# Optimization experiments

Measured on AMD Instinct MI355X. Metric: run time of the kernel, lower is better.

## Reference

```python
import jax, jax.numpy as jnp
import numpy as np

D_MODEL = 4096
N_TYPES = 6  # fixed event_types list in the module


def setup_inputs() -> dict:
    key = jax.random.key(0)
    ks = jax.random.split(key, 7)
    E, B, d = 131072, 16384, D_MODEL
    return {
        "event_type": jax.random.randint(ks[0], (E,), 0, N_TYPES),
        "confidence": jax.random.uniform(ks[1], (E,), jnp.float32),
        "location": jax.random.uniform(ks[2], (E, 2), jnp.float32) * jnp.array([640.0, 480.0], jnp.float32),
        "batch_idx": jax.random.randint(ks[3], (E,), 0, B),
        "batch_size": B,
        "type_emb": jax.random.normal(ks[4], (N_TYPES, d // 4), jnp.float32),
        "W1": jax.random.normal(ks[5], (d // 2, d // 4 + 3), jnp.float32) / np.sqrt(d // 4 + 3).astype(np.float32),
        "b1": jnp.zeros((d // 2,), jnp.float32),
        "W2": jax.random.normal(ks[6], (d, d // 2), jnp.float32) / np.sqrt(d // 2).astype(np.float32),
        "b2": jnp.zeros((d,), jnp.float32),
    }


def reference(event_type, confidence, location, batch_idx, batch_size, type_emb, W1, b1, W2, b2):
    E = confidence.shape[0]
    B = batch_size
    # per-batch-slot max confidence (empty slots -> -inf)
    seg_max = jax.ops.segment_max(confidence, batch_idx, num_segments=B)
    is_top = confidence == seg_max[batch_idx]
    # first event attaining the max (matches torch's max-over-list semantics)
    cand = jnp.where(is_top, jnp.arange(E), E)
    top_idx = jnp.full((B,), E, dtype=cand.dtype).at[batch_idx].min(cand)
    has_event = top_idx < E
    safe_idx = jnp.where(has_event, top_idx, 0)

    emb = type_emb[event_type[safe_idx]]                 # [B, d/4]
    c = confidence[safe_idx][:, None]                    # [B, 1]
    loc = location[safe_idx] / jnp.array([640.0, 480.0], jnp.float32)  # [B, 2]
    feats = jnp.concatenate([emb, c, loc], axis=-1)      # [B, d/4 + 3]

    h = jax.nn.relu(feats @ W1.T + b1)                   # [B, d/2]
    out = h @ W2.T + b2                                  # [B, d]
    return jnp.where(has_event[:, None], out, jnp.zeros((), out.dtype))
```

## Files before the change

kernel.cpp:

```cpp
#include <hip/hip_runtime.h>
#include <hip/hip_bf16.h>

#define NT 6
#define BM 256
#define BN 256
#define BK 64
#define SLOT_S 32768
#define AH1 8192
#define BOFF_A 16384
#define BH1 24576

typedef __attribute__((ext_vector_type(16))) float f32x16;
typedef __attribute__((ext_vector_type(8))) short bf16x8;

__device__ __forceinline__ short f2bf(float f) {
    __hip_bfloat16 h = __float2bfloat16(f);
    return (short)__builtin_bit_cast(unsigned short, h);
}

__global__ void k_segmax(const float* __restrict__ conf,
                         const int* __restrict__ bidx,
                         unsigned long long* __restrict__ packed, int E) {
    int i = blockIdx.x * blockDim.x + threadIdx.x;
    if (i >= E) return;
    unsigned cb = __float_as_uint(conf[i]);
    unsigned long long p = ((unsigned long long)cb << 32) | (unsigned)(~(unsigned)i);
    atomicMax(&packed[bidx[i]], p);
}

__global__ void k_base(const float* __restrict__ emb, const float* __restrict__ W1,
                       const float* __restrict__ b1, float* __restrict__ base,
                       float* __restrict__ vecs, int d2, int d4) {
    int gw = (blockIdx.x * blockDim.x + threadIdx.x) >> 6;
    int lane = threadIdx.x & 63;
    int t = gw / d2, n = gw % d2;
    const float* e = emb + (size_t)t * d4;
    const float* w = W1 + (size_t)n * (d4 + 3);
    float s = 0.f;
    for (int k = lane; k < d4; k += 64) s += e[k] * w[k];
#pragma unroll
    for (int m = 32; m; m >>= 1) s += __shfl_xor(s, m);
    if (lane == 0) {
        base[gw] = s + b1[n];
        if (t == 0) {
            vecs[n]          = w[d4];
            vecs[d2 + n]     = w[d4 + 1];
            vecs[2 * d2 + n] = w[d4 + 2];
        }
    }
}

__global__ void k_w2cast(const float* __restrict__ W2, short* __restrict__ W2b, long n) {
    long i = ((long)blockIdx.x * blockDim.x + threadIdx.x) * 8;
    if (i >= n) return;
    bf16x8 v;
#pragma unroll
    for (int j = 0; j < 8; ++j) v[j] = f2bf(W2[i + j]);
    *(bf16x8*)(W2b + i) = v;
}

__global__ void k_h(const unsigned long long* __restrict__ packed,
                    const int* __restrict__ etype, const float* __restrict__ loc,
                    const float* __restrict__ base, const float* __restrict__ vecs,
                    float* __restrict__ mask, short* __restrict__ h, int d2) {
    int b = blockIdx.x;
    int tid = threadIdx.x;
    unsigned long long p = packed[b];
    bool has = (p != 0ULL);
    float conf = 0.f, lx = 0.f, ly = 0.f;
    int t = 0;
    if (has) {
        unsigned idx = ~(unsigned)(p & 0xFFFFFFFFu);
        conf = __uint_as_float((unsigned)(p >> 32));
        t  = etype[idx];
        lx = loc[2 * (size_t)idx]     * (1.0f / 640.0f);
        ly = loc[2 * (size_t)idx + 1] * (1.0f / 480.0f);
    }
    if (tid == 0) mask[b] = has ? 1.0f : 0.0f;
    const float* bs = base + (size_t)t * d2;
    const float* cv = vecs;
    const float* xv = vecs + d2;
    const float* yv = vecs + 2 * d2;
    int n0 = tid * 8;
    bf16x8 v;
#pragma unroll
    for (int j = 0; j < 8; ++j) {
        int n = n0 + j;
        float g = bs[n] + conf * cv[n] + lx * xv[n] + ly * yv[n];
        g = fmaxf(g, 0.f);
        v[j] = has ? f2bf(g) : (short)0;
    }
    *(bf16x8*)(h + (size_t)b * d2 + n0) = v;
}


#define GLL(src, dst) __builtin_amdgcn_global_load_lds(                      \
    (const __attribute__((address_space(1))) void*)(src),                    \
    (__attribute__((address_space(3))) void*)(dst), 16, 0, 0)

#define ST_AH0(ws, kt) { GLL(pA + (size_t)(kt) * 64, (ws) + dst1);           \
                         GLL(pA + (size_t)64 * K + (kt) * 64, (ws) + dst2); }
#define ST_AH1(ws, kt) { GLL(pA + (size_t)128 * K + (kt) * 64, (ws) + AH1 + dst1); \
                         GLL(pA + (size_t)192 * K + (kt) * 64, (ws) + AH1 + dst2); }
#define ST_BH0(ws, kt) { GLL(pB + (size_t)(kt) * 64, (ws) + BOFF_A + dst1);  \
                         GLL(pB + (size_t)64 * K + (kt) * 64, (ws) + BOFF_A + dst2); }
#define ST_BH1(ws, kt) { GLL(pB + (size_t)128 * K + (kt) * 64, (ws) + BH1 + dst1); \
                         GLL(pB + (size_t)192 * K + (kt) * 64, (ws) + BH1 + dst2); }

__global__ __launch_bounds__(512, 2)
void k_gemm(const short* __restrict__ A, const short* __restrict__ Bm,
            const float* __restrict__ b2, const float* __restrict__ mask,
            float* __restrict__ C, int M, int N, int K, int nbn) {
    __shared__ __align__(16) short lds[2 * SLOT_S];

    int tid = threadIdx.x;
    int lane = tid & 63;
    int wave = tid >> 6;
    int wr = wave >> 2, wc = wave & 3;

    int bid = blockIdx.x;
    int wg = (bid & 7) * ((int)gridDim.x >> 3) + (bid >> 3);
    int bm = wg / nbn, bn = wg % nbn;
    int row0 = bm * BM, col0 = bn * BN;

    int r1 = tid >> 3;
    int pg = tid & 7;
    int cg = pg ^ (r1 & 7);
    const short* pA = A + (size_t)(row0 + r1) * K + cg * 8;
    const short* pB = Bm + (size_t)(col0 + r1) * K + cg * 8;
    int dst1 = tid * 8;
    int dst2 = 4096 + tid * 8;

    int l31 = lane & 31, kh = lane >> 5;
    int kx7 = l31 & 7;
    int aBase = (wr * 128 + l31) * 64;
    int bBase = BOFF_A + (wc * 64 + l31) * 64;
    int coff[4];
#pragma unroll
    for (int s = 0; s < 4; ++s) coff[s] = ((2 * s + kh) ^ kx7) * 8;

    f32x16 acc[4][2] = {};
    bf16x8 aA[4][4], bB[2][4];

    int KT = K / BK;

    ST_AH0(lds, 0); ST_BH0(lds, 0); ST_BH1(lds, 0); ST_AH1(lds, 0);
    asm volatile("s_waitcnt vmcnt(0)" ::: "memory");
    __builtin_amdgcn_s_barrier();

#pragma unroll 1
    for (int t = 0; t < KT; ++t) {
        const short* sl = lds + (t & 1) * SLOT_S;
        short* wsl = lds + ((t + 1) & 1) * SLOT_S;

#pragma unroll
        for (int mi = 0; mi < 4; ++mi)
#pragma unroll
            for (int s = 0; s < 4; ++s)
                aA[mi][s] = *(const bf16x8*)(sl + aBase + mi * 2048 + coff[s]);
#pragma unroll
        for (int ni = 0; ni < 2; ++ni)
#pragma unroll
            for (int s = 0; s < 4; ++s)
                bB[ni][s] = *(const bf16x8*)(sl + bBase + ni * 2048 + coff[s]);

        if (t < KT - 1) {
            ST_AH0(wsl, t + 1); ST_BH0(wsl, t + 1);
            ST_BH1(wsl, t + 1); ST_AH1(wsl, t + 1);
        }

        __builtin_amdgcn_s_setprio(1);
#pragma unroll
        for (int mi = 0; mi < 4; ++mi)
#pragma unroll
            for (int ni = 0; ni < 2; ++ni)
#pragma unroll
                for (int s = 0; s < 4; ++s)
                    acc[mi][ni] = __builtin_amdgcn_mfma_f32_32x32x16_bf16(
                        aA[mi][s], bB[ni][s], acc[mi][ni], 0, 0, 0);
        __builtin_amdgcn_s_setprio(0);

        if (t < KT - 1) {
            asm volatile("s_waitcnt vmcnt(0)" ::: "memory");
            __builtin_amdgcn_s_barrier();
        }
    }

#pragma unroll
    for (int mi = 0; mi < 4; ++mi) {
        int rb = row0 + wr * 128 + mi * 32 + 4 * kh;
#pragma unroll
        for (int q = 0; q < 4; ++q) {
#pragma unroll
            for (int j = 0; j < 4; ++j) {
                int r = rb + 8 * q + j;
                float mk = mask[r];
#pragma unroll
                for (int ni = 0; ni < 2; ++ni) {
                    int c = col0 + wc * 64 + ni * 32 + l31;
                    C[(size_t)r * N + c] = (acc[mi][ni][q * 4 + j] + b2[c]) * mk;
                }
            }
        }
    }
}

extern "C" void kernel_launch(void* const* d_in, const int* in_sizes, int n_in,
                              void* d_out, int out_size, void* d_ws, size_t ws_size,
                              hipStream_t stream) {
    const int* etype   = (const int*)d_in[0];
    const float* conf  = (const float*)d_in[1];
    const float* loc   = (const float*)d_in[2];
    const int* bidx    = (const int*)d_in[3];
    const float* emb   = (const float*)d_in[5];
    const float* W1    = (const float*)d_in[6];
    const float* b1    = (const float*)d_in[7];
    const float* W2    = (const float*)d_in[8];
    const float* b2    = (const float*)d_in[9];
    float* out = (float*)d_out;

    int E  = in_sizes[0];
    int d2 = in_sizes[7];
    int d  = in_sizes[9];
    int d4 = in_sizes[5] / NT;
    int B  = out_size / d;

    char* ws = (char*)d_ws;
    unsigned long long* packed = (unsigned long long*)ws;
    float* mask = (float*)(ws + (size_t)B * 8);
    float* base = mask + B;
    float* vecs = base + NT * d2;
    short* w2b  = (short*)(vecs + 3 * d2);
    short* h    = w2b + (size_t)d * d2;

    hipMemsetAsync(packed, 0, (size_t)B * 8, stream);
    k_segmax<<<(E + 255) / 256, 256, 0, stream>>>(conf, bidx, packed, E);
    k_base<<<(NT * d2) / 4, 256, 0, stream>>>(emb, W1, b1, base, vecs, d2, d4);
    long nw2 = (long)d * d2;
    k_w2cast<<<(int)(nw2 / 8 / 256), 256, 0, stream>>>(W2, w2b, nw2);
    k_h<<<B, 256, 0, stream>>>(packed, etype, loc, base, vecs, mask, h, d2);
    int nbm = B / BM, nbn = d / BN;
    k_gemm<<<dim3(nbm * nbn), dim3(512), 0, stream>>>(h, w2b, b2, mask, out, B, d, d2, nbn);
}
```

Measured before the change: 330.9 us.

## Store GEMM tiles in MFMA fragment order in LDS instead of XOR swizzle

Changes how global_load_lds places the A and B tiles in shared memory. Each wave's 64 lanes now write a contiguous 32-row by 16-column fragment, so the MFMA operand reads become linear lane*8 offsets with no XOR swizzle arithmetic and no bank conflicts. It also drops the s_setprio raise around the MFMA block. Global loads now read 64 bytes per row per wave instead of full 128-byte row segments, which may reduce coalescing efficiency.

```diff
diff --git a/kernel.cpp b/kernel.cpp
--- a/kernel.cpp
+++ b/kernel.cpp
@@ -6,9 +6,7 @@
 #define BN 256
 #define BK 64
 #define SLOT_S 32768
-#define AH1 8192
-#define BOFF_A 16384
-#define BH1 24576
+#define B_BASE 16384
 
 typedef __attribute__((ext_vector_type(16))) float f32x16;
 typedef __attribute__((ext_vector_type(8))) short bf16x8;
@@ -98,14 +96,16 @@
     (const __attribute__((address_space(1))) void*)(src),                    \
     (__attribute__((address_space(3))) void*)(dst), 16, 0, 0)
 
-#define ST_AH0(ws, kt) { GLL(pA + (size_t)(kt) * 64, (ws) + dst1);           \
-                         GLL(pA + (size_t)64 * K + (kt) * 64, (ws) + dst2); }
-#define ST_AH1(ws, kt) { GLL(pA + (size_t)128 * K + (kt) * 64, (ws) + AH1 + dst1); \
-                         GLL(pA + (size_t)192 * K + (kt) * 64, (ws) + AH1 + dst2); }
-#define ST_BH0(ws, kt) { GLL(pB + (size_t)(kt) * 64, (ws) + BOFF_A + dst1);  \
-                         GLL(pB + (size_t)64 * K + (kt) * 64, (ws) + BOFF_A + dst2); }
-#define ST_BH1(ws, kt) { GLL(pB + (size_t)128 * K + (kt) * 64, (ws) + BH1 + dst1); \
-                         GLL(pB + (size_t)192 * K + (kt) * 64, (ws) + BH1 + dst2); }
+#define ST_A(ws, kt) {                                                       \
+    GLL(pA + (size_t)(kt) * 64,               (ws) + dstG);                  \
+    GLL(pA + (size_t)64  * K + (kt) * 64,     (ws) + 4096  + dstG);          \
+    GLL(pA + (size_t)128 * K + (kt) * 64,     (ws) + 8192  + dstG);          \
+    GLL(pA + (size_t)192 * K + (kt) * 64,     (ws) + 12288 + dstG); }
+#define ST_B(ws, kt) {                                                       \
+    GLL(pB + (size_t)(kt) * 64,               (ws) + B_BASE + dstG);         \
+    GLL(pB + (size_t)64  * K + (kt) * 64,     (ws) + B_BASE + 4096  + dstG); \
+    GLL(pB + (size_t)128 * K + (kt) * 64,     (ws) + B_BASE + 8192  + dstG); \
+    GLL(pB + (size_t)192 * K + (kt) * 64,     (ws) + B_BASE + 12288 + dstG); }
 
 __global__ __launch_bounds__(512, 2)
 void k_gemm(const short* __restrict__ A, const short* __restrict__ Bm,
@@ -123,28 +123,22 @@
     int bm = wg / nbn, bn = wg % nbn;
     int row0 = bm * BM, col0 = bn * BN;
 
-    int r1 = tid >> 3;
-    int pg = tid & 7;
-    int cg = pg ^ (r1 & 7);
-    const short* pA = A + (size_t)(row0 + r1) * K + cg * 8;
-    const short* pB = Bm + (size_t)(col0 + r1) * K + cg * 8;
-    int dst1 = tid * 8;
-    int dst2 = 4096 + tid * 8;
+    int rA = ((tid >> 8) << 5) + (tid & 31);
+    int cA = (((tid >> 6) & 3) << 1) + ((tid >> 5) & 1);
+    const short* pA = A + (size_t)(row0 + rA) * K + cA * 8;
+    const short* pB = Bm + (size_t)(col0 + rA) * K + cA * 8;
+    int dstG = tid * 8;
 
     int l31 = lane & 31, kh = lane >> 5;
-    int kx7 = l31 & 7;
-    int aBase = (wr * 128 + l31) * 64;
-    int bBase = BOFF_A + (wc * 64 + l31) * 64;
-    int coff[4];
-#pragma unroll
-    for (int s = 0; s < 4; ++s) coff[s] = ((2 * s + kh) ^ kx7) * 8;
+    int aBase = (wr * 4) * 2048 + lane * 8;
+    int bBase = B_BASE + (wc * 2) * 2048 + lane * 8;
 
     f32x16 acc[4][2] = {};
     bf16x8 aA[4][4], bB[2][4];
 
     int KT = K / BK;
 
-    ST_AH0(lds, 0); ST_BH0(lds, 0); ST_BH1(lds, 0); ST_AH1(lds, 0);
+    ST_A(lds, 0); ST_B(lds, 0);
     asm volatile("s_waitcnt vmcnt(0)" ::: "memory");
     __builtin_amdgcn_s_barrier();
 
@@ -157,19 +151,15 @@
         for (int mi = 0; mi < 4; ++mi)
 #pragma unroll
             for (int s = 0; s < 4; ++s)
-                aA[mi][s] = *(const bf16x8*)(sl + aBase + mi * 2048 + coff[s]);
+                aA[mi][s] = *(const bf16x8*)(sl + aBase + mi * 2048 + s * 512);
 #pragma unroll
         for (int ni = 0; ni < 2; ++ni)
 #pragma unroll
             for (int s = 0; s < 4; ++s)
-                bB[ni][s] = *(const bf16x8*)(sl + bBase + ni * 2048 + coff[s]);
-
-        if (t < KT - 1) {
-            ST_AH0(wsl, t + 1); ST_BH0(wsl, t + 1);
-            ST_BH1(wsl, t + 1); ST_AH1(wsl, t + 1);
-        }
-
-        __builtin_amdgcn_s_setprio(1);
+                bB[ni][s] = *(const bf16x8*)(sl + bBase + ni * 2048 + s * 512);
+
+        if (t < KT - 1) { ST_A(wsl, t + 1); ST_B(wsl, t + 1); }
+
 #pragma unroll
         for (int mi = 0; mi < 4; ++mi)
 #pragma unroll
@@ -178,7 +168,6 @@
                 for (int s = 0; s < 4; ++s)
                     acc[mi][ni] = __builtin_amdgcn_mfma_f32_32x32x16_bf16(
                         aA[mi][s], bB[ni][s], acc[mi][ni], 0, 0, 0);
-        __builtin_amdgcn_s_setprio(0);
 
         if (t < KT - 1) {
             asm volatile("s_waitcnt vmcnt(0)" ::: "memory");
```

Result: slower. 421.2 us (+27.3%).
